# Performance work log

Measured on AMD Instinct MI355X. Metric: run time of the kernel, lower is better.

## Reference

```python
import jax, jax.numpy as jnp
import numpy as np

N_NODES = 100000
N_EDGES = 1600000
IN_DIM, HID_DIM, OUT_DIM = 128, 128, 40
EPS = 1e-12


def setup_inputs() -> dict:
    key = jax.random.key(0)
    ks = jax.random.split(key, 7)
    x = jax.random.normal(ks[0], (N_NODES, IN_DIM), dtype=jnp.float32)
    edge_index = jax.random.randint(ks[1], (2, N_EDGES), 0, N_NODES, dtype=jnp.int64)
    s1 = 1.0 / np.sqrt(IN_DIM)
    s2 = 1.0 / np.sqrt(HID_DIM)
    return {
        "x": x,
        "edge_index": edge_index,
        "W1_l": jax.random.normal(ks[2], (HID_DIM, IN_DIM), dtype=jnp.float32) * s1,
        "b1": jnp.zeros((HID_DIM,), dtype=jnp.float32),
        "W1_r": jax.random.normal(ks[3], (HID_DIM, IN_DIM), dtype=jnp.float32) * s1,
        "W2_l": jax.random.normal(ks[4], (OUT_DIM, HID_DIM), dtype=jnp.float32) * s2,
        "b2": jnp.zeros((OUT_DIM,), dtype=jnp.float32),
        "W2_r": jax.random.normal(ks[5], (OUT_DIM, HID_DIM), dtype=jnp.float32) * s2,
    }


def _mean_aggregate(x, src, dst, deg_inv):
    # gather source features, scatter-sum into destination nodes, divide by degree
    summed = jax.ops.segment_sum(x[src], dst, num_segments=N_NODES)  # [N, d]
    return summed * deg_inv[:, None]


def _sage_conv(x, src, dst, deg_inv, W_l, b_l, W_r):
    # PyG SAGEConv(mean, normalize=True): lin_l(mean(x_j)) + lin_r(x_i), then L2-normalize
    agg = _mean_aggregate(x, src, dst, deg_inv)
    out = agg @ W_l.T + b_l + x @ W_r.T
    norm = jnp.sqrt(jnp.sum(out * out, axis=-1, keepdims=True))
    return out / jnp.maximum(norm, EPS)


def reference(x, edge_index, W1_l, b1, W1_r, W2_l, b2, W2_r):
    src, dst = edge_index[0], edge_index[1]
    deg = jax.ops.segment_sum(jnp.ones((src.shape[0],), dtype=x.dtype), dst,
                              num_segments=N_NODES)
    deg_inv = 1.0 / jnp.maximum(deg, 1.0)

    h = _sage_conv(x, src, dst, deg_inv, W1_l, b1, W1_r)
    h = jax.nn.relu(h)  # dropout = identity (deterministic reference)
    h = _sage_conv(h, src, dst, deg_inv, W2_l, b2, W2_r)
    h = jax.nn.relu(h)
    return jax.nn.log_softmax(h, axis=-1)
```

## Files before the change

kernel.cpp:

```cpp
#include <hip/hip_runtime.h>
#include <hip/hip_bf16.h>

#define N_NODES 100000
#define N_EDGES 1600000
#define IN_DIM 128
#define HID_DIM 128
#define OUT_DIM 40

#define BSHIFT 9
#define NBUCK 196
#define CHUNK 4096
#define NCHUNK ((N_EDGES + CHUNK - 1) / CHUNK)

typedef __attribute__((ext_vector_type(8))) short short8;
typedef __attribute__((ext_vector_type(4))) float float4v;
typedef __attribute__((ext_vector_type(2))) unsigned int u32x2;
typedef __attribute__((ext_vector_type(4))) unsigned int u32x4;

typedef unsigned short u16;
typedef unsigned int u32;
typedef unsigned long long u64;

__device__ __forceinline__ float bflo(u32 v) { union { u32 u; float f; } c; c.u = v << 16; return c.f; }
__device__ __forceinline__ float bfhi(u32 v) { union { u32 u; float f; } c; c.u = v & 0xffff0000u; return c.f; }
__device__ __forceinline__ float bf1(u16 v) { union { u32 u; float f; } c; c.u = ((u32)v) << 16; return c.f; }
__device__ __forceinline__ u16 f2bf(float f) {
    union { float f; u32 u; } c; c.f = f;
    u32 r = c.u + 0x7fffu + ((c.u >> 16) & 1u);
    return (u16)(r >> 16);
}
__device__ __forceinline__ u32 pk(float lo, float hi) {
    return ((u32)f2bf(hi) << 16) | (u32)f2bf(lo);
}


#define XBLKS ((N_NODES * IN_DIM / 4 + 255) / 256)
#define WTRIP1 2048
#define WTRIP2 768
#define WBLKS 22

__global__ __launch_bounds__(256) void k_cvtall(
    const float* __restrict__ x, u16* __restrict__ xb,
    const float* __restrict__ w1l, const float* __restrict__ w1r,
    const float* __restrict__ w2l, const float* __restrict__ w2r,
    u16* __restrict__ w1lf, u16* __restrict__ w1rf,
    u16* __restrict__ w2lf, u16* __restrict__ w2rf,
    const int* __restrict__ idx, int* __restrict__ bucket_size) {
    __shared__ int cnt[NBUCK];
    int b = blockIdx.x;
    if (b < XBLKS) {
        int i = b * 256 + threadIdx.x;
        if (i < N_NODES * IN_DIM / 4) {
            float4v v = reinterpret_cast<const float4v*>(x)[i];
            u32x2 o;
            o.x = pk(v.x, v.y);
            o.y = pk(v.z, v.w);
            reinterpret_cast<u32x2*>(xb)[i] = o;
        }
        return;
    }
    if (b < XBLKS + WBLKS) {
        int i = (b - XBLKS) * 256 + threadIdx.x;
        const float* s; u16* d; int t; int rows;
        if (i < WTRIP1)            { s = w1l; d = w1lf; t = i;                 rows = HID_DIM; }
        else if (i < 2*WTRIP1)     { s = w1r; d = w1rf; t = i - WTRIP1;        rows = HID_DIM; }
        else if (i < 2*WTRIP1+WTRIP2)   { s = w2l; d = w2lf; t = i - 2*WTRIP1; rows = OUT_DIM; }
        else if (i < 2*WTRIP1+2*WTRIP2) { s = w2r; d = w2rf; t = i - 2*WTRIP1-WTRIP2; rows = OUT_DIM; }
        else return;
        int lane = t & 63;
        int ks = (t >> 6) & 3;
        int ct = t >> 8;
        int row = ct * 16 + (lane & 15);
        int col = ks * 32 + (lane >> 4) * 8;
        u32x4 o;
        if (row < rows) {
            const float* sp = s + row * 128 + col;
            float4v v0 = *reinterpret_cast<const float4v*>(sp);
            float4v v1 = *reinterpret_cast<const float4v*>(sp + 4);
            o.x = pk(v0.x, v0.y); o.y = pk(v0.z, v0.w);
            o.z = pk(v1.x, v1.y); o.w = pk(v1.z, v1.w);
        } else { o.x = 0; o.y = 0; o.z = 0; o.w = 0; }
        reinterpret_cast<u32x4*>(d)[t] = o;
        return;
    }
    int t = threadIdx.x;
    for (int i = t; i < NBUCK; i += 256) cnt[i] = 0;
    __syncthreads();
    int base = (b - XBLKS - WBLKS) * CHUNK;
    int n = min(CHUNK, N_EDGES - base);
    for (int i = t; i < n; i += 256)
        atomicAdd(&cnt[idx[N_EDGES + base + i] >> BSHIFT], 1);
    __syncthreads();
    for (int i = t; i < NBUCK; i += 256)
        if (cnt[i]) atomicAdd(&bucket_size[i], cnt[i]);
}


__global__ __launch_bounds__(256) void k_bscan(const int* __restrict__ bucket_size,
                                               int* __restrict__ bucket_base,
                                               int* __restrict__ bucket_cur) {
    __shared__ int sa[256], sb[256];
    int t = threadIdx.x;
    int v = (t < NBUCK) ? bucket_size[t] : 0;
    sa[t] = v;
    __syncthreads();
    int *s = sa, *d = sb;
    for (int dd = 1; dd < 256; dd <<= 1) {
        d[t] = s[t] + ((t >= dd) ? s[t - dd] : 0);
        __syncthreads();
        int* tm = s; s = d; d = tm;
    }
    if (t < NBUCK) {
        int base = s[t] - v;
        bucket_base[t] = base;
        bucket_cur[t] = base;
    }
}

__global__ __launch_bounds__(1024) void k_bscatter(const int* __restrict__ idx,
                                                   int* __restrict__ bucket_cur,
                                                   u64* __restrict__ rec) {
    __shared__ int cnt[NBUCK], gbase[NBUCK];
    int t = threadIdx.x;
    const int nt = 1024;
    for (int i = t; i < NBUCK; i += nt) cnt[i] = 0;
    __syncthreads();
    int base = blockIdx.x * CHUNK;
    int n = min(CHUNK, N_EDGES - base);
    int eb[4], eq[4];
    u64 er[4];
    #pragma unroll
    for (int k = 0; k < 4; ++k) {
        int i = t + k * nt;
        if (i < n) {
            int srcv = idx[base + i];
            int dstv = idx[N_EDGES + base + i];
            int b = dstv >> BSHIFT;
            eb[k] = b;
            eq[k] = atomicAdd(&cnt[b], 1);
            er[k] = ((u64)(u32)dstv << 32) | (u32)srcv;
        }
    }
    __syncthreads();
    for (int i = t; i < NBUCK; i += nt) {
        int v = cnt[i];
        gbase[i] = v ? atomicAdd(&bucket_cur[i], v) : 0;
    }
    __syncthreads();
    #pragma unroll
    for (int k = 0; k < 4; ++k) {
        int i = t + k * nt;
        if (i < n) rec[gbase[eb[k]] + eq[k]] = er[k];
    }
}

__global__ __launch_bounds__(1024) void k_bfill(const u64* __restrict__ rec,
                                                const int* __restrict__ bucket_base,
                                                const int* __restrict__ bucket_size,
                                                int* __restrict__ row_start,
                                                int* __restrict__ csr) {
    __shared__ int deg[512], cur[512];
    __shared__ int sa[512], sb[512];
    int t = threadIdx.x;
    int nt = blockDim.x;
    int b = blockIdx.x;
    int node0 = b << BSHIFT;
    int nn = min(512, N_NODES - node0);
    int ebase = bucket_base[b];
    int esz = bucket_size[b];
    for (int i = t; i < 512; i += nt) deg[i] = 0;
    __syncthreads();
    for (int i = t; i < esz; i += nt)
        atomicAdd(&deg[((int)(rec[ebase + i] >> 32)) & 511], 1);
    __syncthreads();
    for (int i = t; i < 512; i += nt) sa[i] = deg[i];
    __syncthreads();
    int *s = sa, *d = sb;
    for (int dd = 1; dd < 512; dd <<= 1) {
        for (int i = t; i < 512; i += nt) d[i] = s[i] + ((i >= dd) ? s[i - dd] : 0);
        __syncthreads();
        int* tm = s; s = d; d = tm;
    }
    for (int i = t; i < 512; i += nt) {
        int excl = s[i] - deg[i];
        cur[i] = excl;
        if (i < nn) row_start[node0 + i] = ebase + excl;
    }
    if (b == NBUCK - 1 && t == 0) row_start[N_NODES] = N_EDGES;
    __syncthreads();
    for (int i = t; i < esz; i += nt) {
        u64 r = rec[ebase + i];
        int dl = ((int)(r >> 32)) & 511;
        int p = atomicAdd(&cur[dl], 1);
        csr[ebase + p] = (int)(r & 0xffffffffu);
    }
}


__global__ void k_agg(const u16* __restrict__ feat,
                      const int* __restrict__ csr,
                      const int* __restrict__ row_start,
                      u16* __restrict__ agg) {
    int n = blockIdx.x * 4 + (threadIdx.x >> 6);
    int lane = threadIdx.x & 63;
    if (n >= N_NODES) return;
    int s = row_start[n];
    int e = row_start[n + 1];
    int half = lane >> 5;
    int li = lane & 31;
    const u32x2* fp = reinterpret_cast<const u32x2*>(feat);
    float a0 = 0.f, a1 = 0.f, a2 = 0.f, a3 = 0.f;
    int p = s;
    int i0 = 0, i1 = 0, i2 = 0, i3 = 0;
    if (p + 8 <= e) {
        i0 = csr[p + half];     i1 = csr[p + 2 + half];
        i2 = csr[p + 4 + half]; i3 = csr[p + 6 + half];
    }
    while (p + 8 <= e) {
        u32x2 v0 = fp[i0 * 32 + li];
        u32x2 v1 = fp[i1 * 32 + li];
        u32x2 v2 = fp[i2 * 32 + li];
        u32x2 v3 = fp[i3 * 32 + li];
        p += 8;
        if (p + 8 <= e) {
            i0 = csr[p + half];     i1 = csr[p + 2 + half];
            i2 = csr[p + 4 + half]; i3 = csr[p + 6 + half];
        }
        a0 += bflo(v0.x) + bflo(v1.x) + bflo(v2.x) + bflo(v3.x);
        a1 += bfhi(v0.x) + bfhi(v1.x) + bfhi(v2.x) + bfhi(v3.x);
        a2 += bflo(v0.y) + bflo(v1.y) + bflo(v2.y) + bflo(v3.y);
        a3 += bfhi(v0.y) + bfhi(v1.y) + bfhi(v2.y) + bfhi(v3.y);
    }
    for (; p + 2 <= e; p += 2) {
        int i = csr[p + half];
        u32x2 v = fp[i * 32 + li];
        a0 += bflo(v.x); a1 += bfhi(v.x);
        a2 += bflo(v.y); a3 += bfhi(v.y);
    }
    if (p < e && half == 0) {
        int i = csr[p];
        u32x2 v = fp[i * 32 + li];
        a0 += bflo(v.x); a1 += bfhi(v.x);
        a2 += bflo(v.y); a3 += bfhi(v.y);
    }
    a0 += __shfl_xor(a0, 32);
    a1 += __shfl_xor(a1, 32);
    a2 += __shfl_xor(a2, 32);
    a3 += __shfl_xor(a3, 32);
    if (half == 0) {
        float sc = 1.0f / (float)max(e - s, 1);
        u32x2 o;
        o.x = pk(a0 * sc, a1 * sc);
        o.y = pk(a2 * sc, a3 * sc);
        reinterpret_cast<u32x2*>(agg)[n * 32 + li] = o;
    }
}


__global__ __launch_bounds__(256) void k_dense1(
    const u16* __restrict__ agg, const u16* __restrict__ x,
    const u16* __restrict__ W1lf, const u16* __restrict__ W1rf,
    const float* __restrict__ b1, u16* __restrict__ h) {
    __shared__ short8 wsh[2][WTRIP1];
    int t = threadIdx.x;
    int wave = t >> 6;
    int lane = t & 63;
    int nb = blockIdx.x * 64 + wave * 16;
    int q = lane >> 4;
    int m = lane & 15;
    int arow = nb + m;
    if (arow >= N_NODES) arow = N_NODES - 1;

    short8 afr[8];
    #pragma unroll
    for (int ks = 0; ks < 4; ++ks) {
        afr[ks]     = *reinterpret_cast<const short8*>(agg + arow * 128 + ks * 32 + q * 8);
        afr[4 + ks] = *reinterpret_cast<const short8*>(x   + arow * 128 + ks * 32 + q * 8);
    }
    const short8* g0 = reinterpret_cast<const short8*>(W1lf);
    const short8* g1 = reinterpret_cast<const short8*>(W1rf);
    #pragma unroll
    for (int k = 0; k < 8; ++k) {
        wsh[0][t + k * 256] = g0[t + k * 256];
        wsh[1][t + k * 256] = g1[t + k * 256];
    }
    __syncthreads();

    float4v acc[8];
    #pragma unroll
    for (int ct = 0; ct < 8; ++ct) acc[ct] = (float4v){0.f, 0.f, 0.f, 0.f};

    #pragma unroll
    for (int half = 0; half < 2; ++half)
        #pragma unroll
        for (int ks = 0; ks < 4; ++ks) {
            short8 a = afr[half * 4 + ks];
            #pragma unroll
            for (int ct = 0; ct < 8; ++ct) {
                short8 b = wsh[half][(ct * 4 + ks) * 64 + lane];
                acc[ct] = __builtin_amdgcn_mfma_f32_16x16x32_bf16(a, b, acc[ct], 0, 0, 0);
            }
        }

    float bias[8];
    #pragma unroll
    for (int ct = 0; ct < 8; ++ct) bias[ct] = b1[ct * 16 + m];

    float nsq[4] = { 0.f, 0.f, 0.f, 0.f };
    #pragma unroll
    for (int ct = 0; ct < 8; ++ct)
        #pragma unroll
        for (int r = 0; r < 4; ++r) {
            float v = acc[ct][r] + bias[ct];
            acc[ct][r] = v;
            nsq[r] += v * v;
        }
    #pragma unroll
    for (int r = 0; r < 4; ++r) {
        float tt = nsq[r];
        tt += __shfl_xor(tt, 1);
        tt += __shfl_xor(tt, 2);
        tt += __shfl_xor(tt, 4);
        tt += __shfl_xor(tt, 8);
        nsq[r] = 1.0f / fmaxf(sqrtf(tt), 1e-12f);
    }
    #pragma unroll
    for (int r = 0; r < 4; ++r) {
        int node = nb + q * 4 + r;
        if (node < N_NODES) {
            #pragma unroll
            for (int ct = 0; ct < 8; ++ct) {
                float v = fmaxf(acc[ct][r] * nsq[r], 0.0f);
                h[node * 128 + ct * 16 + m] = f2bf(v);
            }
        }
    }
}


__global__ __launch_bounds__(256) void k_dense2a(
    const u16* __restrict__ h,
    const u16* __restrict__ W2lf, const u16* __restrict__ W2rf,
    u16* __restrict__ y2, u16* __restrict__ z) {
    __shared__ short8 wsh[2][WTRIP2];
    int t = threadIdx.x;
    int wave = t >> 6;
    int lane = t & 63;
    int nb = blockIdx.x * 64 + wave * 16;
    int q = lane >> 4;
    int m = lane & 15;
    int arow = nb + m;
    if (arow >= N_NODES) arow = N_NODES - 1;

    short8 afr[4];
    #pragma unroll
    for (int ks = 0; ks < 4; ++ks)
        afr[ks] = *reinterpret_cast<const short8*>(h + arow * 128 + ks * 32 + q * 8);
    const short8* g0 = reinterpret_cast<const short8*>(W2lf);
    const short8* g1 = reinterpret_cast<const short8*>(W2rf);
    #pragma unroll
    for (int k = 0; k < 3; ++k) {
        wsh[0][t + k * 256] = g0[t + k * 256];
        wsh[1][t + k * 256] = g1[t + k * 256];
    }
    __syncthreads();

    float4v accl[3], accr[3];
    #pragma unroll
    for (int ct = 0; ct < 3; ++ct) {
        accl[ct] = (float4v){0.f, 0.f, 0.f, 0.f};
        accr[ct] = (float4v){0.f, 0.f, 0.f, 0.f};
    }
    #pragma unroll
    for (int ks = 0; ks < 4; ++ks) {
        short8 a = afr[ks];
        #pragma unroll
        for (int ct = 0; ct < 3; ++ct) {
            accl[ct] = __builtin_amdgcn_mfma_f32_16x16x32_bf16(a, wsh[0][(ct * 4 + ks) * 64 + lane], accl[ct], 0, 0, 0);
            accr[ct] = __builtin_amdgcn_mfma_f32_16x16x32_bf16(a, wsh[1][(ct * 4 + ks) * 64 + lane], accr[ct], 0, 0, 0);
        }
    }
    #pragma unroll
    for (int r = 0; r < 4; ++r) {
        int node = nb + q * 4 + r;
        if (node < N_NODES) {
            #pragma unroll
            for (int ct = 0; ct < 3; ++ct) {
                int col = ct * 16 + m;
                y2[node * 64 + col] = f2bf(accl[ct][r]);
                z[node * 48 + col]  = f2bf(accr[ct][r]);
            }
            y2[node * 64 + 48 + m] = 0;
        }
    }
}


__global__ void k_agg2(const u16* __restrict__ y2,
                       const int* __restrict__ csr,
                       const int* __restrict__ row_start,
                       const u16* __restrict__ z,
                       const float* __restrict__ b2,
                       float* __restrict__ out) {
    int n = blockIdx.x * 4 + (threadIdx.x >> 6);
    int lane = threadIdx.x & 63;
    if (n >= N_NODES) return;
    int s = row_start[n];
    int e = row_start[n + 1];
    int g = lane >> 4;
    int li = lane & 15;
    const u32x2* fp = reinterpret_cast<const u32x2*>(y2);
    float a0 = 0.f, a1 = 0.f, a2 = 0.f, a3 = 0.f;
    float zb0 = 0.f, zb1 = 0.f, zb2 = 0.f, zb3 = 0.f;
    if (li < 10) {
        u32x2 zv = *reinterpret_cast<const u32x2*>(z + n * 48 + li * 4);
        float4v bv = *reinterpret_cast<const float4v*>(b2 + li * 4);
        zb0 = bflo(zv.x) + bv.x; zb1 = bfhi(zv.x) + bv.y;
        zb2 = bflo(zv.y) + bv.z; zb3 = bfhi(zv.y) + bv.w;
    }
    int p = s;
    int i0 = 0, i1 = 0;
    if (p + 8 <= e) { i0 = csr[p + g]; i1 = csr[p + 4 + g]; }
    while (p + 8 <= e) {
        u32x2 v0 = fp[i0 * 16 + li];
        u32x2 v1 = fp[i1 * 16 + li];
        p += 8;
        if (p + 8 <= e) { i0 = csr[p + g]; i1 = csr[p + 4 + g]; }
        a0 += bflo(v0.x) + bflo(v1.x);
        a1 += bfhi(v0.x) + bfhi(v1.x);
        a2 += bflo(v0.y) + bflo(v1.y);
        a3 += bfhi(v0.y) + bfhi(v1.y);
    }
    if (p + g < e) {
        u32x2 v = fp[csr[p + g] * 16 + li];
        a0 += bflo(v.x); a1 += bfhi(v.x);
        a2 += bflo(v.y); a3 += bfhi(v.y);
    }
    if (p + 4 + g < e) {
        u32x2 v = fp[csr[p + 4 + g] * 16 + li];
        a0 += bflo(v.x); a1 += bfhi(v.x);
        a2 += bflo(v.y); a3 += bfhi(v.y);
    }
    a0 += __shfl_xor(a0, 16); a0 += __shfl_xor(a0, 32);
    a1 += __shfl_xor(a1, 16); a1 += __shfl_xor(a1, 32);
    a2 += __shfl_xor(a2, 16); a2 += __shfl_xor(a2, 32);
    a3 += __shfl_xor(a3, 16); a3 += __shfl_xor(a3, 32);

    float sc = 1.0f / (float)max(e - s, 1);
    float v0 = 0.f, v1 = 0.f, v2 = 0.f, v3 = 0.f;
    if (li < 10) {
        v0 = a0 * sc + zb0; v1 = a1 * sc + zb1;
        v2 = a2 * sc + zb2; v3 = a3 * sc + zb3;
    }
    float nsq = v0 * v0 + v1 * v1 + v2 * v2 + v3 * v3;
    nsq += __shfl_xor(nsq, 1);
    nsq += __shfl_xor(nsq, 2);
    nsq += __shfl_xor(nsq, 4);
    nsq += __shfl_xor(nsq, 8);
    float rn = 1.0f / fmaxf(sqrtf(nsq), 1e-12f);
    v0 = fmaxf(v0 * rn, 0.f); v1 = fmaxf(v1 * rn, 0.f);
    v2 = fmaxf(v2 * rn, 0.f); v3 = fmaxf(v3 * rn, 0.f);
    float mv = fmaxf(fmaxf(v0, v1), fmaxf(v2, v3));
    mv = fmaxf(mv, __shfl_xor(mv, 1));
    mv = fmaxf(mv, __shfl_xor(mv, 2));
    mv = fmaxf(mv, __shfl_xor(mv, 4));
    mv = fmaxf(mv, __shfl_xor(mv, 8));
    float se = 0.f;
    if (li < 10)
        se = __expf(v0 - mv) + __expf(v1 - mv) + __expf(v2 - mv) + __expf(v3 - mv);
    se += __shfl_xor(se, 1);
    se += __shfl_xor(se, 2);
    se += __shfl_xor(se, 4);
    se += __shfl_xor(se, 8);
    float lse = __logf(se);
    if (g == 0 && li < 10) {
        float4v o = { v0 - mv - lse, v1 - mv - lse, v2 - mv - lse, v3 - mv - lse };
        *reinterpret_cast<float4v*>(out + n * OUT_DIM + li * 4) = o;
    }
}


extern "C" void kernel_launch(void* const* d_in, const int* in_sizes, int n_in,
                              void* d_out, int out_size, void* d_ws, size_t ws_size,
                              hipStream_t stream) {
    const float* x   = (const float*)d_in[0];
    const int*   idx = (const int*)d_in[1];
    const float* W1l = (const float*)d_in[2];
    const float* b1  = (const float*)d_in[3];
    const float* W1r = (const float*)d_in[4];
    const float* W2l = (const float*)d_in[5];
    const float* b2  = (const float*)d_in[6];
    const float* W2r = (const float*)d_in[7];
    float* out = (float*)d_out;

    char* ws = (char*)d_ws;
    int*   bucket_size = (int*)(ws + 0);
    int*   bucket_base = (int*)(ws + 4096);
    int*   bucket_cur  = (int*)(ws + 8192);
    int*   row_start   = (int*)(ws + 16384);
    int*   csr         = (int*)(ws + 1216384);
    u16*   xb          = (u16*)(ws + 7616512);
    u16*   y2          = (u16*)(ws + 7616512);
    u16*   z           = (u16*)(ws + 20416512);
    u16*   agg         = (u16*)(ws + 33216512);
    u16*   h           = (u16*)(ws + 58816512);
    u64*   rec         = (u64*)(ws + 58816512);
    u16*   W1lf        = (u16*)(ws + 84416512);
    u16*   W1rf        = (u16*)(ws + 84449280);
    u16*   W2lf        = (u16*)(ws + 84482048);
    u16*   W2rf        = (u16*)(ws + 84494336);

    hipMemsetAsync(bucket_size, 0, NBUCK * sizeof(int), stream);

    k_cvtall<<<XBLKS + WBLKS + NCHUNK, 256, 0, stream>>>(
        x, xb, W1l, W1r, W2l, W2r, W1lf, W1rf, W2lf, W2rf, idx, bucket_size);

    k_bscan<<<1, 256, 0, stream>>>(bucket_size, bucket_base, bucket_cur);
    k_bscatter<<<NCHUNK, 1024, 0, stream>>>(idx, bucket_cur, rec);
    k_bfill<<<NBUCK, 1024, 0, stream>>>(rec, bucket_base, bucket_size,
                                        row_start, csr);

    k_agg<<<N_NODES / 4, 256, 0, stream>>>(xb, csr, row_start, agg);
    k_dense1<<<(N_NODES + 63) / 64, 256, 0, stream>>>(agg, xb, W1lf, W1rf, b1, h);
    k_dense2a<<<(N_NODES + 63) / 64, 256, 0, stream>>>(h, W2lf, W2rf, y2, z);
    k_agg2<<<N_NODES / 4, 256, 0, stream>>>(y2, csr, row_start, z, b2, out);
}
```

Baseline: 300.0 us.

## Gather layer-1 neighbor features in FP8 and fold bucket scan into scatter/fill

Input features are also quantized to FP8 (e4m3) in the conversion kernel. The first aggregation then gathers 128 bytes per neighbor instead of 256 and decodes them with the hardware packed fp8-to-f32 convert, which cuts gather bandwidth in the memory-bound layer-1 aggregation. Separately, the single-block bucket scan kernel is removed: its prefix sum is recomputed redundantly inside every scatter and fill block, saving one launch. The trade-offs are reduced precision of the aggregated features, which may stress tolerance, and extra FP8 conversion work plus a larger memset.

```diff
diff --git a/kernel.cpp b/kernel.cpp
--- a/kernel.cpp
+++ b/kernel.cpp
@@ -14,6 +14,7 @@
 
 typedef __attribute__((ext_vector_type(8))) short short8;
 typedef __attribute__((ext_vector_type(4))) float float4v;
+typedef __attribute__((ext_vector_type(2))) float f32x2;
 typedef __attribute__((ext_vector_type(2))) unsigned int u32x2;
 typedef __attribute__((ext_vector_type(4))) unsigned int u32x4;
 
@@ -23,7 +24,6 @@
 
 __device__ __forceinline__ float bflo(u32 v) { union { u32 u; float f; } c; c.u = v << 16; return c.f; }
 __device__ __forceinline__ float bfhi(u32 v) { union { u32 u; float f; } c; c.u = v & 0xffff0000u; return c.f; }
-__device__ __forceinline__ float bf1(u16 v) { union { u32 u; float f; } c; c.u = ((u32)v) << 16; return c.f; }
 __device__ __forceinline__ u16 f2bf(float f) {
     union { float f; u32 u; } c; c.f = f;
     u32 r = c.u + 0x7fffu + ((c.u >> 16) & 1u);
@@ -33,6 +33,23 @@
     return ((u32)f2bf(hi) << 16) | (u32)f2bf(lo);
 }
 
+__device__ __forceinline__ u32 f2fp8(float f) {
+    union { float f; u32 u; } c; c.f = f;
+    u32 s = (c.u >> 24) & 0x80u;
+    u32 a = c.u & 0x7fffffffu;
+    u32 code;
+    if (a >= 0x3C800000u) {
+        if (a > 0x43E00000u) a = 0x43E00000u;
+        u32 r = a + 0x0007FFFFu + ((a >> 20) & 1u);
+        code = (((r >> 23) - 120u) << 3) | ((r >> 20) & 7u);
+        if (code > 0x7Eu) code = 0x7Eu;
+    } else {
+        union { u32 u; float f; } d; d.u = a;
+        code = (u32)(int)rintf(d.f * 512.0f);
+    }
+    return s | code;
+}
+
 
 #define XBLKS ((N_NODES * IN_DIM / 4 + 255) / 256)
 #define WTRIP1 2048
@@ -40,7 +57,7 @@
 #define WBLKS 22
 
 __global__ __launch_bounds__(256) void k_cvtall(
-    const float* __restrict__ x, u16* __restrict__ xb,
+    const float* __restrict__ x, u16* __restrict__ xb, u32* __restrict__ xb8,
     const float* __restrict__ w1l, const float* __restrict__ w1r,
     const float* __restrict__ w2l, const float* __restrict__ w2r,
     u16* __restrict__ w1lf, u16* __restrict__ w1rf,
@@ -56,6 +73,7 @@
             o.x = pk(v.x, v.y);
             o.y = pk(v.z, v.w);
             reinterpret_cast<u32x2*>(xb)[i] = o;
+            xb8[i] = f2fp8(v.x) | (f2fp8(v.y) << 8) | (f2fp8(v.z) << 16) | (f2fp8(v.w) << 24);
         }
         return;
     }
@@ -96,31 +114,12 @@
 }
 
 
-__global__ __launch_bounds__(256) void k_bscan(const int* __restrict__ bucket_size,
-                                               int* __restrict__ bucket_base,
-                                               int* __restrict__ bucket_cur) {
-    __shared__ int sa[256], sb[256];
-    int t = threadIdx.x;
-    int v = (t < NBUCK) ? bucket_size[t] : 0;
-    sa[t] = v;
-    __syncthreads();
-    int *s = sa, *d = sb;
-    for (int dd = 1; dd < 256; dd <<= 1) {
-        d[t] = s[t] + ((t >= dd) ? s[t - dd] : 0);
-        __syncthreads();
-        int* tm = s; s = d; d = tm;
-    }
-    if (t < NBUCK) {
-        int base = s[t] - v;
-        bucket_base[t] = base;
-        bucket_cur[t] = base;
-    }
-}
-
 __global__ __launch_bounds__(1024) void k_bscatter(const int* __restrict__ idx,
+                                                   const int* __restrict__ bucket_size,
                                                    int* __restrict__ bucket_cur,
                                                    u64* __restrict__ rec) {
     __shared__ int cnt[NBUCK], gbase[NBUCK];
+    __shared__ int sa[256], sb[256];
     int t = threadIdx.x;
     const int nt = 1024;
     for (int i = t; i < NBUCK; i += nt) cnt[i] = 0;
@@ -141,10 +140,21 @@
             er[k] = ((u64)(u32)dstv << 32) | (u32)srcv;
         }
     }
-    __syncthreads();
-    for (int i = t; i < NBUCK; i += nt) {
-        int v = cnt[i];
-        gbase[i] = v ? atomicAdd(&bucket_cur[i], v) : 0;
+    int myv = 0;
+    if (t < 256) {
+        myv = (t < NBUCK) ? bucket_size[t] : 0;
+        sa[t] = myv;
+    }
+    __syncthreads();
+    int *s = sa, *d = sb;
+    for (int dd = 1; dd < 256; dd <<= 1) {
+        if (t < 256) d[t] = s[t] + ((t >= dd) ? s[t - dd] : 0);
+        __syncthreads();
+        int* tm = s; s = d; d = tm;
+    }
+    if (t < NBUCK) {
+        int v = cnt[t];
+        gbase[t] = v ? (s[t] - myv) + atomicAdd(&bucket_cur[t], v) : 0;
     }
     __syncthreads();
     #pragma unroll
@@ -155,7 +165,6 @@
 }
 
 __global__ __launch_bounds__(1024) void k_bfill(const u64* __restrict__ rec,
-                                                const int* __restrict__ bucket_base,
                                                 const int* __restrict__ bucket_size,
                                                 int* __restrict__ row_start,
                                                 int* __restrict__ csr) {
@@ -166,8 +175,21 @@
     int b = blockIdx.x;
     int node0 = b << BSHIFT;
     int nn = min(512, N_NODES - node0);
-    int ebase = bucket_base[b];
     int esz = bucket_size[b];
+    if (t < 256) sa[t] = (t < NBUCK) ? bucket_size[t] : 0;
+    __syncthreads();
+    {
+        int *s = sa, *d = sb;
+        for (int dd = 1; dd < 256; dd <<= 1) {
+            if (t < 256) d[t] = s[t] + ((t >= dd) ? s[t - dd] : 0);
+            __syncthreads();
+            int* tm = s; s = d; d = tm;
+        }
+        if (t == 0) cur[0] = s[b] - esz;
+    }
+    __syncthreads();
+    int ebase = cur[0];
+    __syncthreads();
     for (int i = t; i < 512; i += nt) deg[i] = 0;
     __syncthreads();
     for (int i = t; i < esz; i += nt)
@@ -197,7 +219,7 @@
 }
 
 
-__global__ void k_agg(const u16* __restrict__ feat,
+__global__ void k_agg(const u32x2* __restrict__ fp,
                       const int* __restrict__ csr,
                       const int* __restrict__ row_start,
                       u16* __restrict__ agg) {
@@ -206,53 +228,47 @@
     if (n >= N_NODES) return;
     int s = row_start[n];
     int e = row_start[n + 1];
-    int half = lane >> 5;
-    int li = lane & 31;
-    const u32x2* fp = reinterpret_cast<const u32x2*>(feat);
+    int g = lane >> 4;
+    int li = lane & 15;
     float a0 = 0.f, a1 = 0.f, a2 = 0.f, a3 = 0.f;
+    float a4 = 0.f, a5 = 0.f, a6 = 0.f, a7 = 0.f;
+#define ACC8(v) do { \
+        f32x2 d_; \
+        d_ = __builtin_amdgcn_cvt_pk_f32_fp8((v).x, false); a0 += d_.x; a1 += d_.y; \
+        d_ = __builtin_amdgcn_cvt_pk_f32_fp8((v).x, true);  a2 += d_.x; a3 += d_.y; \
+        d_ = __builtin_amdgcn_cvt_pk_f32_fp8((v).y, false); a4 += d_.x; a5 += d_.y; \
+        d_ = __builtin_amdgcn_cvt_pk_f32_fp8((v).y, true);  a6 += d_.x; a7 += d_.y; \
+    } while (0)
     int p = s;
-    int i0 = 0, i1 = 0, i2 = 0, i3 = 0;
-    if (p + 8 <= e) {
-        i0 = csr[p + half];     i1 = csr[p + 2 + half];
-        i2 = csr[p + 4 + half]; i3 = csr[p + 6 + half];
-    }
+    int i0 = 0, i1 = 0;
+    if (p + 8 <= e) { i0 = csr[p + g]; i1 = csr[p + 4 + g]; }
     while (p + 8 <= e) {
-        u32x2 v0 = fp[i0 * 32 + li];
-        u32x2 v1 = fp[i1 * 32 + li];
-        u32x2 v2 = fp[i2 * 32 + li];
-        u32x2 v3 = fp[i3 * 32 + li];
+        u32x2 v0 = fp[i0 * 16 + li];
+        u32x2 v1 = fp[i1 * 16 + li];
         p += 8;
-        if (p + 8 <= e) {
-            i0 = csr[p + half];     i1 = csr[p + 2 + half];
-            i2 = csr[p + 4 + half]; i3 = csr[p + 6 + half];
-        }
-        a0 += bflo(v0.x) + bflo(v1.x) + bflo(v2.x) + bflo(v3.x);
-        a1 += bfhi(v0.x) + bfhi(v1.x) + bfhi(v2.x) + bfhi(v3.x);
-        a2 += bflo(v0.y) + bflo(v1.y) + bflo(v2.y) + bflo(v3.y);
-        a3 += bfhi(v0.y) + bfhi(v1.y) + bfhi(v2.y) + bfhi(v3.y);
-    }
-    for (; p + 2 <= e; p += 2) {
-        int i = csr[p + half];
-        u32x2 v = fp[i * 32 + li];
-        a0 += bflo(v.x); a1 += bfhi(v.x);
-        a2 += bflo(v.y); a3 += bfhi(v.y);
-    }
-    if (p < e && half == 0) {
-        int i = csr[p];
-        u32x2 v = fp[i * 32 + li];
-        a0 += bflo(v.x); a1 += bfhi(v.x);
-        a2 += bflo(v.y); a3 += bfhi(v.y);
-    }
-    a0 += __shfl_xor(a0, 32);
-    a1 += __shfl_xor(a1, 32);
-    a2 += __shfl_xor(a2, 32);
-    a3 += __shfl_xor(a3, 32);
-    if (half == 0) {
+        if (p + 8 <= e) { i0 = csr[p + g]; i1 = csr[p + 4 + g]; }
+        ACC8(v0);
+        ACC8(v1);
+    }
+    if (p + g < e) { u32x2 v = fp[csr[p + g] * 16 + li]; ACC8(v); }
+    if (p + 4 + g < e) { u32x2 v = fp[csr[p + 4 + g] * 16 + li]; ACC8(v); }
+#undef ACC8
+    a0 += __shfl_xor(a0, 16); a0 += __shfl_xor(a0, 32);
+    a1 += __shfl_xor(a1, 16); a1 += __shfl_xor(a1, 32);
+    a2 += __shfl_xor(a2, 16); a2 += __shfl_xor(a2, 32);
+    a3 += __shfl_xor(a3, 16); a3 += __shfl_xor(a3, 32);
+    a4 += __shfl_xor(a4, 16); a4 += __shfl_xor(a4, 32);
+    a5 += __shfl_xor(a5, 16); a5 += __shfl_xor(a5, 32);
+    a6 += __shfl_xor(a6, 16); a6 += __shfl_xor(a6, 32);
+    a7 += __shfl_xor(a7, 16); a7 += __shfl_xor(a7, 32);
+    if (g == 0) {
         float sc = 1.0f / (float)max(e - s, 1);
-        u32x2 o;
+        u32x4 o;
         o.x = pk(a0 * sc, a1 * sc);
         o.y = pk(a2 * sc, a3 * sc);
-        reinterpret_cast<u32x2*>(agg)[n * 32 + li] = o;
+        o.z = pk(a4 * sc, a5 * sc);
+        o.w = pk(a6 * sc, a7 * sc);
+        *reinterpret_cast<u32x4*>(agg + n * 128 + li * 8) = o;
     }
 }
 
@@ -495,32 +511,30 @@
 
     char* ws = (char*)d_ws;
     int*   bucket_size = (int*)(ws + 0);
-    int*   bucket_base = (int*)(ws + 4096);
-    int*   bucket_cur  = (int*)(ws + 8192);
+    int*   bucket_cur  = (int*)(ws + 1024);
     int*   row_start   = (int*)(ws + 16384);
     int*   csr         = (int*)(ws + 1216384);
     u16*   xb          = (u16*)(ws + 7616512);
     u16*   y2          = (u16*)(ws + 7616512);
     u16*   z           = (u16*)(ws + 20416512);
     u16*   agg         = (u16*)(ws + 33216512);
+    u64*   rec         = (u64*)(ws + 58816512);
+    u32*   xb8         = (u32*)(ws + 71616512);
     u16*   h           = (u16*)(ws + 58816512);
-    u64*   rec         = (u64*)(ws + 58816512);
     u16*   W1lf        = (u16*)(ws + 84416512);
     u16*   W1rf        = (u16*)(ws + 84449280);
     u16*   W2lf        = (u16*)(ws + 84482048);
     u16*   W2rf        = (u16*)(ws + 84494336);
 
-    hipMemsetAsync(bucket_size, 0, NBUCK * sizeof(int), stream);
+    hipMemsetAsync(ws, 0, 1808, stream);
 
     k_cvtall<<<XBLKS + WBLKS + NCHUNK, 256, 0, stream>>>(
-        x, xb, W1l, W1r, W2l, W2r, W1lf, W1rf, W2lf, W2rf, idx, bucket_size);
-
-    k_bscan<<<1, 256, 0, stream>>>(bucket_size, bucket_base, bucket_cur);
-    k_bscatter<<<NCHUNK, 1024, 0, stream>>>(idx, bucket_cur, rec);
-    k_bfill<<<NBUCK, 1024, 0, stream>>>(rec, bucket_base, bucket_size,
-                                        row_start, csr);
-
-    k_agg<<<N_NODES / 4, 256, 0, stream>>>(xb, csr, row_start, agg);
+        x, xb, xb8, W1l, W1r, W2l, W2r, W1lf, W1rf, W2lf, W2rf, idx, bucket_size);
+
+    k_bscatter<<<NCHUNK, 1024, 0, stream>>>(idx, bucket_size, bucket_cur, rec);
+    k_bfill<<<NBUCK, 1024, 0, stream>>>(rec, bucket_size, row_start, csr);
+
+    k_agg<<<N_NODES / 4, 256, 0, stream>>>((const u32x2*)xb8, csr, row_start, agg);
     k_dense1<<<(N_NODES + 63) / 64, 256, 0, stream>>>(agg, xb, W1lf, W1rf, b1, h);
     k_dense2a<<<(N_NODES + 63) / 64, 256, 0, stream>>>(h, W2lf, W2rf, y2, z);
     k_agg2<<<N_NODES / 4, 256, 0, stream>>>(y2, csr, row_start, z, b2, out);
```

After: 284.5 us. -5.2%, faster.
